# Kernel optimization log

Hardware: AMD Instinct MI355X
Metric: run time of the kernel (lower is better)

## Reference

```python
import jax, jax.numpy as jnp
import numpy as np

BATCH = 2048
INPUT_DIM = 256
NUM_SUBCARRIERS = 256
HIDDEN_DIM = 256


def setup_inputs() -> dict:
    key = jax.random.key(0)
    ks = jax.random.split(key, 7)
    C, I, H = NUM_SUBCARRIERS, INPUT_DIM, HIDDEN_DIM
    # PyTorch nn.Linear default init: U(-1/sqrt(fan_in), 1/sqrt(fan_in))
    s1 = 1.0 / np.sqrt(I)
    s2 = 1.0 / np.sqrt(H)
    x = jax.random.normal(ks[0], (BATCH, I), dtype=jnp.float32)
    W1 = jax.random.uniform(ks[1], (C, I, H), jnp.float32, -s1, s1)
    b1 = jax.random.uniform(ks[2], (C, H), jnp.float32, -s1, s1)
    W2 = jax.random.uniform(ks[3], (C, H, H), jnp.float32, -s2, s2)
    b2 = jax.random.uniform(ks[4], (C, H), jnp.float32, -s2, s2)
    W3 = jax.random.uniform(ks[5], (C, H), jnp.float32, -s2, s2)  # [C, H] (out dim 1 squeezed)
    b3 = jax.random.uniform(ks[6], (C,), jnp.float32, -s2, s2)
    return {"x": x, "W1": W1, "b1": b1, "W2": W2, "b2": b2, "W3": W3, "b3": b3}


def reference(x, W1, b1, W2, b2, W3, b3):
    # Stacked (batched) version of the per-subcarrier Python loop:
    # for each subcarrier c: relu(relu(x @ W1[c] + b1[c]) @ W2[c] + b2[c]) @ W3[c] + b3[c]
    h1 = jax.nn.relu(jnp.einsum('bi,cih->cbh', x, W1) + b1[:, None, :])   # [C, B, H]
    h2 = jax.nn.relu(jnp.einsum('cbh,chk->cbk', h1, W2) + b2[:, None, :])  # [C, B, H]
    out = jnp.einsum('cbh,ch->cb', h2, W3) + b3[:, None]                   # [C, B]
    return out.T  # [B, C], matches torch.cat(outputs, dim=1)
```

## Files before the change

kernel.cpp:

```cpp
#include <hip/hip_runtime.h>

typedef unsigned short u16;
using u16x4  = __attribute__((ext_vector_type(4))) unsigned short;
using u16x8  = __attribute__((ext_vector_type(8))) unsigned short;
using bf16x8 = __attribute__((ext_vector_type(8))) short;
using f32x4  = __attribute__((ext_vector_type(4))) float;
using f32x16 = __attribute__((ext_vector_type(16))) float;

__device__ __forceinline__ u16 f2bf(float f) {
  union { float f; unsigned u; } v; v.f = f;
  unsigned r = v.u + 0x7FFFu + ((v.u >> 16) & 1u);
  return (u16)(r >> 16);
}

__device__ __forceinline__ unsigned cvt_pk_bf16(float a, float b) {
  unsigned d;
  asm("v_cvt_pk_bf16_f32 %0, %1, %2" : "=v"(d) : "v"(a), "v"(b));
  return d;
}

__global__ __launch_bounds__(256) void prepass_k(
    const float* __restrict__ W1, const float* __restrict__ W2,
    u16* __restrict__ w1t, u16* __restrict__ w2t,
    const float* __restrict__ x, u16* __restrict__ xb) {
  __shared__ float tile[64][65];
  const int bid = blockIdx.x;
  const int t = threadIdx.x;
  if (bid >= 8192) {
    int i = (bid - 8192) * 256 + t;
    float4 v = ((const float4*)x)[i];
    u16x4 u;
    u.x = f2bf(v.x); u.y = f2bf(v.y); u.z = f2bf(v.z); u.w = f2bf(v.w);
    ((u16x4*)xb)[i] = u;
    return;
  }
  const int mat = bid >> 4;
  const int tl  = bid & 15;
  const int i0 = (tl >> 2) * 64, h0 = (tl & 3) * 64;
  const float* src = (mat < 256) ? (W1 + mat * 65536) : (W2 + (mat - 256) * 65536);
  u16*       dst   = (mat < 256) ? (w1t + mat * 65536) : (w2t + (mat - 256) * 65536);
#pragma unroll
  for (int j = 0; j < 4; ++j) {
    int lin = j * 256 + t;
    int row = lin >> 4, c4 = lin & 15;
    float4 v = *(const float4*)(src + (i0 + row) * 256 + h0 + c4 * 4);
    tile[row][c4 * 4 + 0] = v.x; tile[row][c4 * 4 + 1] = v.y;
    tile[row][c4 * 4 + 2] = v.z; tile[row][c4 * 4 + 3] = v.w;
  }
  __syncthreads();
  const int col = t >> 2;
  const int kk  = (t & 3) * 8;
#pragma unroll
  for (int p = 0; p < 2; ++p) {
    u16x8 o;
#pragma unroll
    for (int jj = 0; jj < 8; ++jj)
      o[jj] = f2bf(tile[p * 32 + kk + jj][col]);
    *(u16x8*)(dst + ((i0 >> 4) + 2 * p + (kk >> 4)) * 4096 + (h0 + col) * 16 + (kk & 8)) = o;
  }
}

__global__ __launch_bounds__(512, 2) void rf_main_k(
    const u16* __restrict__ xb, const u16* __restrict__ w1t, const u16* __restrict__ w2t,
    const float* __restrict__ b1, const float* __restrict__ b2,
    const float* __restrict__ w3, const float* __restrict__ b3,
    float* __restrict__ out) {
  __shared__ u16 sH[256 * 264];

  const int bid  = blockIdx.x;
  const int xcd  = bid & 7;
  const int j8   = bid >> 3;
  const int c    = xcd * 32 + (j8 >> 3);
  const int b0   = (j8 & 7) * 256;
  const int t    = threadIdx.x;
  const int lane = t & 63;
  const int w    = t >> 6;
  const int l31  = lane & 31;
  const int hi   = lane >> 5;
  const bool hiH = hi != 0;
  const int wq   = w & 3;
  const int bh   = w >> 2;
  const int m_base = wq * 64;

  const u16* w1c = w1t + c * 65536;
  const u16* w2c = w2t + c * 65536;
  const int aoff = (m_base + l31) * 16 + hi * 8;
  int bb[4];
#pragma unroll
  for (int nj = 0; nj < 4; ++nj)
    bb[nj] = (bh * 128 + nj * 32 + l31) * 264 + hi * 8;
  const int bidx = __builtin_amdgcn_readfirstlane(c * 256 + m_base);

  f32x16 acc[2][4];
  bf16x8 aA[2], aB[2], bX[4], bY[4];

#define LOADA(dst, base)                                         \
  { dst[0] = *(const bf16x8*)(base);                             \
    dst[1] = *(const bf16x8*)((base) + 512); }

#define LOADB(dst, ch)                                           \
  { _Pragma("unroll")                                            \
    for (int _nj = 0; _nj < 4; ++_nj)                            \
      dst[_nj] = *(const bf16x8*)&sH[bb[_nj] + (ch) * 16]; }

#define COMPUTE(afr, bfr)                                        \
  { _Pragma("unroll")                                            \
    for (int _nj = 0; _nj < 4; ++_nj) {                          \
      acc[0][_nj] = __builtin_amdgcn_mfma_f32_32x32x16_bf16(afr[0], bfr[_nj], acc[0][_nj], 0, 0, 0); \
      acc[1][_nj] = __builtin_amdgcn_mfma_f32_32x32x16_bf16(afr[1], bfr[_nj], acc[1][_nj], 0, 0, 0); \
    } }

#define INIT_ACC(bp)                                             \
  { _Pragma("unroll")                                            \
    for (int _mi = 0; _mi < 2; ++_mi) {                          \
      _Pragma("unroll")                                          \
      for (int _g = 0; _g < 4; ++_g) {                           \
        f32x4 _lo = *(const f32x4*)((bp) + bidx + _mi * 32 + _g * 8);     \
        f32x4 _h4 = *(const f32x4*)((bp) + bidx + _mi * 32 + _g * 8 + 4); \
        _Pragma("unroll")                                        \
        for (int _r = 0; _r < 4; ++_r) {                         \
          float _v = hiH ? _h4[_r] : _lo[_r];                    \
          _Pragma("unroll")                                      \
          for (int _nj = 0; _nj < 4; ++_nj)                      \
            acc[_mi][_nj][_g * 4 + _r] = _v;                     \
        } } } }

  LOADA(aA, w1c + aoff);

#pragma unroll
  for (int i = 0; i < 16; ++i) {
    int flat = i * 512 + t;
    int r = flat >> 5, s = flat & 31;
    u16x8 g = *(const u16x8*)(xb + (b0 + r) * 256 + s * 8);
    *(u16x8*)&sH[r * 264 + s * 8] = g;
  }
  INIT_ACC(b1);
  __syncthreads();

  LOADB(bX, 0);
#pragma unroll 1
  for (int ch = 0; ch < 16; ch += 2) {
    LOADA(aB, w1c + (ch + 1) * 4096 + aoff);
    LOADB(bY, ch + 1);
    COMPUTE(aA, bX);
    const u16* nxt = (ch == 14) ? (w2c + aoff)
                                : (w1c + (ch + 2) * 4096 + aoff);
    LOADA(aA, nxt);
    if (ch < 14) LOADB(bX, ch + 2);
    COMPUTE(aB, bY);
  }

  __syncthreads();
#pragma unroll
  for (int nj = 0; nj < 4; ++nj) {
    const int row = bh * 128 + nj * 32 + l31;
#pragma unroll
    for (int mi = 0; mi < 2; ++mi)
#pragma unroll
      for (int g = 0; g < 4; ++g) {
        float v0 = fmaxf(acc[mi][nj][g * 4 + 0], 0.f);
        float v1 = fmaxf(acc[mi][nj][g * 4 + 1], 0.f);
        float v2 = fmaxf(acc[mi][nj][g * 4 + 2], 0.f);
        float v3 = fmaxf(acc[mi][nj][g * 4 + 3], 0.f);
        uint2 p;
        p.x = cvt_pk_bf16(v0, v1);
        p.y = cvt_pk_bf16(v2, v3);
        *(uint2*)&sH[row * 264 + m_base + mi * 32 + g * 8 + 4 * hi] = p;
      }
  }
  INIT_ACC(b2);
  __syncthreads();

  LOADB(bX, 0);
#pragma unroll 1
  for (int ch = 0; ch < 16; ch += 2) {
    LOADA(aB, w2c + (ch + 1) * 4096 + aoff);
    LOADB(bY, ch + 1);
    COMPUTE(aA, bX);
    if (ch < 14) {
      LOADA(aA, w2c + (ch + 2) * 4096 + aoff);
      LOADB(bX, ch + 2);
    }
    COMPUTE(aB, bY);
  }

  float part[4] = {0.f, 0.f, 0.f, 0.f};
#pragma unroll
  for (int mi = 0; mi < 2; ++mi)
#pragma unroll
    for (int g = 0; g < 4; ++g) {
      f32x4 wlo = *(const f32x4*)(w3 + bidx + mi * 32 + g * 8);
      f32x4 whi = *(const f32x4*)(w3 + bidx + mi * 32 + g * 8 + 4);
#pragma unroll
      for (int r = 0; r < 4; ++r) {
        float wv = hiH ? whi[r] : wlo[r];
#pragma unroll
        for (int nj = 0; nj < 4; ++nj)
          part[nj] += fmaxf(acc[mi][nj][g * 4 + r], 0.f) * wv;
      }
    }
  __syncthreads();
  float* red = (float*)sH;
#pragma unroll
  for (int nj = 0; nj < 4; ++nj)
    red[(wq * 2 + hi) * 256 + bh * 128 + nj * 32 + l31] = part[nj];
  __syncthreads();
  if (t < 256) {
    float v = b3[c];
#pragma unroll
    for (int k = 0; k < 8; ++k) v += red[k * 256 + t];
    out[(b0 + t) * 256 + c] = v;
  }
#undef LOADA
#undef LOADB
#undef COMPUTE
#undef INIT_ACC
}

extern "C" void kernel_launch(void* const* d_in, const int* in_sizes, int n_in,
                              void* d_out, int out_size, void* d_ws, size_t ws_size,
                              hipStream_t stream) {
  const float* x  = (const float*)d_in[0];
  const float* W1 = (const float*)d_in[1];
  const float* b1 = (const float*)d_in[2];
  const float* W2 = (const float*)d_in[3];
  const float* b2 = (const float*)d_in[4];
  const float* W3 = (const float*)d_in[5];
  const float* b3 = (const float*)d_in[6];
  float* out = (float*)d_out;

  char* ws = (char*)d_ws;
  u16* xb  = (u16*)ws;
  u16* w1t = (u16*)(ws + (1u << 20));
  u16* w2t = (u16*)(ws + (1u << 20) + (32u << 20));

  prepass_k <<<8704, 256, 0, stream>>>(W1, W2, w1t, w2t, x, xb);
  rf_main_k <<<2048, 512, 0, stream>>>(xb, w1t, w2t, b1, b2, W3, b3, out);
}
```

Before: 302.3 us.

## Deepen weight prefetch to a 4-stage ring and fold b2 into epilogue

```diff
diff --git a/kernel.cpp b/kernel.cpp
--- a/kernel.cpp
+++ b/kernel.cpp
@@ -92,7 +92,8 @@
   const int bidx = __builtin_amdgcn_readfirstlane(c * 256 + m_base);
 
   f32x16 acc[2][4];
-  bf16x8 aA[2], aB[2], bX[4], bY[4];
+  bf16x8 aS[4][2];
+  bf16x8 bS[2][4];
 
 #define LOADA(dst, base)                                         \
   { dst[0] = *(const bf16x8*)(base);                             \
@@ -110,22 +111,9 @@
       acc[1][_nj] = __builtin_amdgcn_mfma_f32_32x32x16_bf16(afr[1], bfr[_nj], acc[1][_nj], 0, 0, 0); \
     } }
 
-#define INIT_ACC(bp)                                             \
-  { _Pragma("unroll")                                            \
-    for (int _mi = 0; _mi < 2; ++_mi) {                          \
-      _Pragma("unroll")                                          \
-      for (int _g = 0; _g < 4; ++_g) {                           \
-        f32x4 _lo = *(const f32x4*)((bp) + bidx + _mi * 32 + _g * 8);     \
-        f32x4 _h4 = *(const f32x4*)((bp) + bidx + _mi * 32 + _g * 8 + 4); \
-        _Pragma("unroll")                                        \
-        for (int _r = 0; _r < 4; ++_r) {                         \
-          float _v = hiH ? _h4[_r] : _lo[_r];                    \
-          _Pragma("unroll")                                      \
-          for (int _nj = 0; _nj < 4; ++_nj)                      \
-            acc[_mi][_nj][_g * 4 + _r] = _v;                     \
-        } } } }
-
-  LOADA(aA, w1c + aoff);
+  LOADA(aS[0], w1c + 0 * 4096 + aoff);
+  LOADA(aS[1], w1c + 1 * 4096 + aoff);
+  LOADA(aS[2], w1c + 2 * 4096 + aoff);
 
 #pragma unroll
   for (int i = 0; i < 16; ++i) {
@@ -134,20 +122,29 @@
     u16x8 g = *(const u16x8*)(xb + (b0 + r) * 256 + s * 8);
     *(u16x8*)&sH[r * 264 + s * 8] = g;
   }
-  INIT_ACC(b1);
-  __syncthreads();
-
-  LOADB(bX, 0);
-#pragma unroll 1
-  for (int ch = 0; ch < 16; ch += 2) {
-    LOADA(aB, w1c + (ch + 1) * 4096 + aoff);
-    LOADB(bY, ch + 1);
-    COMPUTE(aA, bX);
-    const u16* nxt = (ch == 14) ? (w2c + aoff)
-                                : (w1c + (ch + 2) * 4096 + aoff);
-    LOADA(aA, nxt);
-    if (ch < 14) LOADB(bX, ch + 2);
-    COMPUTE(aB, bY);
+#pragma unroll
+  for (int mi = 0; mi < 2; ++mi)
+#pragma unroll
+    for (int g = 0; g < 4; ++g) {
+      f32x4 lo = *(const f32x4*)(b1 + bidx + mi * 32 + g * 8);
+      f32x4 h4 = *(const f32x4*)(b1 + bidx + mi * 32 + g * 8 + 4);
+#pragma unroll
+      for (int r = 0; r < 4; ++r) {
+        float v = hiH ? h4[r] : lo[r];
+#pragma unroll
+        for (int nj = 0; nj < 4; ++nj)
+          acc[mi][nj][g * 4 + r] = v;
+      }
+    }
+  __syncthreads();
+
+  LOADB(bS[0], 0);
+#pragma unroll
+  for (int ch = 0; ch < 16; ++ch) {
+    const u16* ab = (ch + 3 < 16) ? (w1c + (ch + 3) * 4096) : (w2c + (ch - 13) * 4096);
+    LOADA(aS[(ch + 3) & 3], ab + aoff);
+    if (ch + 1 < 16) LOADB(bS[(ch + 1) & 1], ch + 1);
+    COMPUTE(aS[ch & 3], bS[ch & 1]);
   }
 
   __syncthreads();
@@ -166,22 +163,18 @@
         p.x = cvt_pk_bf16(v0, v1);
         p.y = cvt_pk_bf16(v2, v3);
         *(uint2*)&sH[row * 264 + m_base + mi * 32 + g * 8 + 4 * hi] = p;
+        acc[mi][nj][g * 4 + 0] = 0.f; acc[mi][nj][g * 4 + 1] = 0.f;
+        acc[mi][nj][g * 4 + 2] = 0.f; acc[mi][nj][g * 4 + 3] = 0.f;
       }
   }
-  INIT_ACC(b2);
-  __syncthreads();
-
-  LOADB(bX, 0);
-#pragma unroll 1
-  for (int ch = 0; ch < 16; ch += 2) {
-    LOADA(aB, w2c + (ch + 1) * 4096 + aoff);
-    LOADB(bY, ch + 1);
-    COMPUTE(aA, bX);
-    if (ch < 14) {
-      LOADA(aA, w2c + (ch + 2) * 4096 + aoff);
-      LOADB(bX, ch + 2);
-    }
-    COMPUTE(aB, bY);
+  __syncthreads();
+
+  LOADB(bS[0], 0);
+#pragma unroll
+  for (int ch = 0; ch < 16; ++ch) {
+    if (ch + 3 < 16) LOADA(aS[(ch + 3) & 3], w2c + (ch + 3) * 4096 + aoff);
+    if (ch + 1 < 16) LOADB(bS[(ch + 1) & 1], ch + 1);
+    COMPUTE(aS[ch & 3], bS[ch & 1]);
   }
 
   float part[4] = {0.f, 0.f, 0.f, 0.f};
@@ -189,14 +182,17 @@
   for (int mi = 0; mi < 2; ++mi)
 #pragma unroll
     for (int g = 0; g < 4; ++g) {
+      f32x4 blo = *(const f32x4*)(b2 + bidx + mi * 32 + g * 8);
+      f32x4 bh4 = *(const f32x4*)(b2 + bidx + mi * 32 + g * 8 + 4);
       f32x4 wlo = *(const f32x4*)(w3 + bidx + mi * 32 + g * 8);
-      f32x4 whi = *(const f32x4*)(w3 + bidx + mi * 32 + g * 8 + 4);
+      f32x4 wh4 = *(const f32x4*)(w3 + bidx + mi * 32 + g * 8 + 4);
 #pragma unroll
       for (int r = 0; r < 4; ++r) {
-        float wv = hiH ? whi[r] : wlo[r];
+        float bv = hiH ? bh4[r] : blo[r];
+        float wv = hiH ? wh4[r] : wlo[r];
 #pragma unroll
         for (int nj = 0; nj < 4; ++nj)
-          part[nj] += fmaxf(acc[mi][nj][g * 4 + r], 0.f) * wv;
+          part[nj] += fmaxf(acc[mi][nj][g * 4 + r] + bv, 0.f) * wv;
       }
     }
   __syncthreads();
@@ -214,7 +210,6 @@
 #undef LOADA
 #undef LOADB
 #undef COMPUTE
-#undef INIT_ACC
 }
 
 extern "C" void kernel_launch(void* const* d_in, const int* in_sizes, int n_in,
```

New measurement: 301.7 us. No clear change (-0.2%).
